# Kernel optimization log

Hardware: AMD Instinct MI355X
Metric: run time of the kernel (lower is better)

Reference implementation:

```python
import jax, jax.numpy as jnp
import numpy as np

DIM = 768
HEADS = 12
HIDDEN = int(DIM * 4.0)


def layernorm(x, w, b, eps=1e-5):
    mu = jnp.mean(x, axis=-1, keepdims=True)
    var = jnp.var(x, axis=-1, keepdims=True)
    return (x - mu) * jax.lax.rsqrt(var + eps) * w + b


def setup_inputs() -> dict:
    key = jax.random.key(0)
    ks = jax.random.split(key, 16)
    B, Nq, Nc, D = 4, 1024, 1024, DIM
    s = 0.02
    return {
        "query_tokens": jax.random.normal(ks[0], (B, Nq, D), jnp.float32),
        "context_tokens": jax.random.normal(ks[1], (B, Nc, D), jnp.float32),
        "wind_bias": jax.random.normal(ks[2], (B, 1, Nq, Nc), jnp.float32),
        "ln_q_w": jnp.ones((D,), jnp.float32), "ln_q_b": jnp.zeros((D,), jnp.float32),
        "ln_kv_w": jnp.ones((D,), jnp.float32), "ln_kv_b": jnp.zeros((D,), jnp.float32),
        "Wq": jax.random.normal(ks[3], (D, D), jnp.float32) * s, "bq": jnp.zeros((D,), jnp.float32),
        "Wk": jax.random.normal(ks[4], (D, D), jnp.float32) * s, "bk": jnp.zeros((D,), jnp.float32),
        "Wv": jax.random.normal(ks[5], (D, D), jnp.float32) * s, "bv": jnp.zeros((D,), jnp.float32),
        "Wo": jax.random.normal(ks[6], (D, D), jnp.float32) * s, "bo": jnp.zeros((D,), jnp.float32),
        "beta": jnp.ones((HEADS, 1, 1), jnp.float32),
        "ln_f_w": jnp.ones((D,), jnp.float32), "ln_f_b": jnp.zeros((D,), jnp.float32),
        "W1": jax.random.normal(ks[7], (D, HIDDEN), jnp.float32) * s, "b1": jnp.zeros((HIDDEN,), jnp.float32),
        "W2": jax.random.normal(ks[8], (HIDDEN, D), jnp.float32) * s, "b2": jnp.zeros((D,), jnp.float32),
    }


def reference(query_tokens, context_tokens, wind_bias,
              ln_q_w, ln_q_b, ln_kv_w, ln_kv_b,
              Wq, bq, Wk, bk, Wv, bv, Wo, bo, beta,
              ln_f_w, ln_f_b, W1, b1, W2, b2):
    B, Nq, D = query_tokens.shape
    H = HEADS
    hd = D // H
    scale = hd ** -0.5

    q = layernorm(query_tokens, ln_q_w, ln_q_b) @ Wq + bq
    kv = layernorm(context_tokens, ln_kv_w, ln_kv_b)
    k = kv @ Wk + bk
    v = kv @ Wv + bv

    # [B, H, N, hd]
    q = q.reshape(B, Nq, H, hd).transpose(0, 2, 1, 3)
    k = k.reshape(B, -1, H, hd).transpose(0, 2, 1, 3)
    v = v.reshape(B, -1, H, hd).transpose(0, 2, 1, 3)

    attn = jnp.einsum('bhqd,bhkd->bhqk', q * scale, k)
    attn = attn + beta * wind_bias  # beta: [H,1,1] broadcasts over [B,H,Nq,Nc]
    attn = jax.nn.softmax(attn.astype(jnp.float32), axis=-1).astype(q.dtype)

    out = jnp.einsum('bhqk,bhkd->bhqd', attn, v).transpose(0, 2, 1, 3).reshape(B, Nq, D)
    out = out @ Wo + bo

    x = query_tokens + out
    h = layernorm(x, ln_f_w, ln_f_b)
    h = jax.nn.gelu(h @ W1 + b1, approximate=False) @ W2 + b2
    return x + h
```

## Files before the change

kernel.cpp:

```cpp
#include <hip/hip_runtime.h>
#include <hip/hip_bf16.h>


#define DIM 768
#define HID 3072
#define NHEAD 12
#define BATCH 4
#define SEQ 1024
#define ROWS (BATCH * SEQ)
#define HD 64

typedef __attribute__((ext_vector_type(8))) __bf16 bf16x8;
typedef __attribute__((ext_vector_type(4))) float f32x4;
typedef __attribute__((ext_vector_type(4))) unsigned int u32x4;
typedef __attribute__((ext_vector_type(2))) unsigned int u32x2;

#define MFMA16(a, b, c) __builtin_amdgcn_mfma_f32_16x16x32_bf16((a), (b), (c), 0, 0, 0)

#define GLDS16(g, l)                                                         \
  __builtin_amdgcn_global_load_lds(                                          \
      (const __attribute__((address_space(1))) void*)(g),                    \
      (__attribute__((address_space(3))) void*)(l), 16, 0, 0)

__device__ __forceinline__ unsigned pk2(float lo, float hi) {
  unsigned a = __bfloat16_as_ushort(__float2bfloat16(lo));
  unsigned b = __bfloat16_as_ushort(__float2bfloat16(hi));
  return a | (b << 16);
}

__global__ __launch_bounds__(256) void wg_transpose4(const float* __restrict__ Wq,
                                                     const float* __restrict__ Wk,
                                                     const float* __restrict__ Wv,
                                                     const float* __restrict__ Wo,
                                                     __hip_bfloat16* __restrict__ WqT,
                                                     __hip_bfloat16* __restrict__ WkT,
                                                     __hip_bfloat16* __restrict__ WvT,
                                                     __hip_bfloat16* __restrict__ WoT) {
  __shared__ float tile[32][33];
  const int z = blockIdx.z;
  const float* W = (z == 0) ? Wq : (z == 1) ? Wk : (z == 2) ? Wv : Wo;
  __hip_bfloat16* WT = (z == 0) ? WqT : (z == 1) ? WkT : (z == 2) ? WvT : WoT;
  const int tx = threadIdx.x & 31, ty = threadIdx.x >> 5;
  const int n0 = blockIdx.x * 32, k0 = blockIdx.y * 32;
#pragma unroll
  for (int i = 0; i < 4; i++)
    tile[ty + i * 8][tx] = W[(size_t)(k0 + ty + i * 8) * DIM + n0 + tx];
  __syncthreads();
#pragma unroll
  for (int i = 0; i < 4; i++)
    WT[(size_t)(n0 + ty + i * 8) * DIM + k0 + tx] = __float2bfloat16(tile[tx][ty + i * 8]);
}

__global__ __launch_bounds__(256) void wg_transpose(const float* __restrict__ W,
                                                    __hip_bfloat16* __restrict__ WT,
                                                    int K, int N) {
  __shared__ float tile[32][33];
  const int tx = threadIdx.x & 31, ty = threadIdx.x >> 5;
  const int n0 = blockIdx.x * 32, k0 = blockIdx.y * 32;
#pragma unroll
  for (int i = 0; i < 4; i++)
    tile[ty + i * 8][tx] = W[(size_t)(k0 + ty + i * 8) * N + n0 + tx];
  __syncthreads();
#pragma unroll
  for (int i = 0; i < 4; i++)
    WT[(size_t)(n0 + ty + i * 8) * K + k0 + tx] = __float2bfloat16(tile[tx][ty + i * 8]);
}

__global__ void wg_bcat(const float* __restrict__ bq, const float* __restrict__ bk,
                        const float* __restrict__ bv, float* __restrict__ bc) {
  int i = blockIdx.x * 256 + threadIdx.x;
  if (i < 768) bc[i] = bq[i];
  else if (i < 1536) bc[i] = bk[i - 768];
  else if (i < 2304) bc[i] = bv[i - 1536];
}

template <int DUAL>
__global__ __launch_bounds__(256) void wg_ln(const float* __restrict__ inA,
                                             const float* __restrict__ wA,
                                             const float* __restrict__ bA,
                                             const float* __restrict__ inB,
                                             const float* __restrict__ wB,
                                             const float* __restrict__ bB,
                                             __hip_bfloat16* __restrict__ outbuf) {
  int row = blockIdx.x;
  int t = threadIdx.x;
  const float* in = inA;
  const float* w = wA;
  const float* b = bA;
  int lrow = row;
  if (DUAL && row >= ROWS) {
    in = inB; w = wB; b = bB; lrow = row - ROWS;
  }
  const float* p = in + (size_t)lrow * DIM;
  float v0 = p[t], v1 = p[t + 256], v2 = p[t + 512];
  float s = v0 + v1 + v2;
  float q = v0 * v0 + v1 * v1 + v2 * v2;
#pragma unroll
  for (int d = 1; d < 64; d <<= 1) {
    s += __shfl_xor(s, d);
    q += __shfl_xor(q, d);
  }
  __shared__ float ss[4], sq[4];
  if ((t & 63) == 0) {
    ss[t >> 6] = s;
    sq[t >> 6] = q;
  }
  __syncthreads();
  s = ss[0] + ss[1] + ss[2] + ss[3];
  q = sq[0] + sq[1] + sq[2] + sq[3];
  float mu = s * (1.0f / DIM);
  float var = q * (1.0f / DIM) - mu * mu;
  float rs = rsqrtf(var + 1e-5f);
  __hip_bfloat16* o = outbuf + (size_t)row * DIM;
  o[t] = __float2bfloat16((v0 - mu) * rs * w[t] + b[t]);
  o[t + 256] = __float2bfloat16((v1 - mu) * rs * w[t + 256] + b[t + 256]);
  o[t + 512] = __float2bfloat16((v2 - mu) * rs * w[t + 512] + b[t + 512]);
}

template <int MODE>
__global__ __launch_bounds__(512) void wg_gemm(const __hip_bfloat16* __restrict__ A,
                                               const __hip_bfloat16* __restrict__ BT,
                                               const float* __restrict__ bias,
                                               void* __restrict__ Cout,
                                               const float* __restrict__ resid,
                                               float* __restrict__ aux,
                                               int N, int Kloop, int Kstride, float p0) {
  __shared__ __hip_bfloat16 As[3][128 * 32];
  __shared__ __hip_bfloat16 Bs[3][128 * 32];
  const int t = threadIdx.x;
  const int lane = t & 63;
  const int wave = t >> 6;
  const int wr = wave >> 1, wc = wave & 1;
  const int lhi = lane >> 4, llo = lane & 15;
  const int nbn = N >> 7;
  const int bm = blockIdx.x / nbn, bn = blockIdx.x % nbn;
  const int koff = (MODE == 7) ? blockIdx.y * Kloop : 0;

  const __hip_bfloat16* Ause = A;
  if (MODE == 6 && bn >= 6) Ause = A + (size_t)ROWS * DIM;

  const int srow = t >> 2;
  const int sg = ((t & 3) ^ ((srow >> 1) & 3)) * 8;
  const __hip_bfloat16* Ag = Ause + (size_t)(bm * 128 + srow) * Kstride + koff + sg;
  const __hip_bfloat16* Bg = BT + (size_t)(bn * 128 + srow) * Kstride + koff + sg;

  f32x4 zero = {0.f, 0.f, 0.f, 0.f};
  f32x4 acc[2][4];
#pragma unroll
  for (int i = 0; i < 2; i++)
#pragma unroll
    for (int j = 0; j < 4; j++) acc[i][j] = zero;

  const int nk = Kloop >> 5;

  GLDS16(Ag, &As[0][t * 8]);
  GLDS16(Bg, &Bs[0][t * 8]);
  GLDS16(Ag + 32, &As[1][t * 8]);
  GLDS16(Bg + 32, &Bs[1][t * 8]);

  int buf = 0;
  for (int kt = 0; kt < nk; kt++) {
    if (kt < nk - 1) {
      asm volatile("s_waitcnt vmcnt(2)" ::: "memory");
    } else {
      asm volatile("s_waitcnt vmcnt(0)" ::: "memory");
    }
    __builtin_amdgcn_s_barrier();
    asm volatile("" ::: "memory");
    if (kt + 2 < nk) {
      int nbuf = buf + 2;
      if (nbuf >= 3) nbuf -= 3;
      GLDS16(Ag + (kt + 2) * 32, &As[nbuf][t * 8]);
      GLDS16(Bg + (kt + 2) * 32, &Bs[nbuf][t * 8]);
    }
    bf16x8 af[2], bfr[4];
#pragma unroll
    for (int i = 0; i < 2; i++) {
      const int row = wr * 32 + i * 16 + llo;
      af[i] = *reinterpret_cast<const bf16x8*>(
          &As[buf][row * 32 + ((lhi ^ ((row >> 1) & 3)) << 3)]);
    }
#pragma unroll
    for (int j = 0; j < 4; j++) {
      const int row = wc * 64 + j * 16 + llo;
      bfr[j] = *reinterpret_cast<const bf16x8*>(
          &Bs[buf][row * 32 + ((lhi ^ ((row >> 1) & 3)) << 3)]);
    }
    __builtin_amdgcn_s_setprio(1);
#pragma unroll
    for (int i = 0; i < 2; i++)
#pragma unroll
      for (int j = 0; j < 4; j++) acc[i][j] = MFMA16(af[i], bfr[j], acc[i][j]);
    __builtin_amdgcn_s_setprio(0);
    buf++;
    if (buf == 3) buf = 0;
  }

#pragma unroll
  for (int i = 0; i < 2; i++) {
    int gr = bm * 128 + wr * 32 + i * 16 + lhi * 4;
#pragma unroll
    for (int j = 0; j < 4; j++) {
      int gc = bn * 128 + wc * 64 + j * 16 + llo;
      float bv_ = (MODE == 7) ? 0.f : bias[gc];
#pragma unroll
      for (int r = 0; r < 4; r++) {
        float v = acc[i][j][r] + bv_;
        int row = gr + r;
        size_t idx = (size_t)row * N + gc;
        if (MODE == 3) {
          aux[idx] = resid[idx] + v;
        } else if (MODE == 4) {
          float x3 = v * v * v;
          float z = -2.302208f * v - 0.102943f * x3;
          float g = v / (1.0f + exp2f(z));
          ((__hip_bfloat16*)Cout)[idx] = __float2bfloat16(g);
        } else if (MODE == 7) {
          aux[(size_t)blockIdx.y * ROWS * N + idx] = v;
        } else if (MODE == 6) {
          int sec = gc / 768;
          int n2 = gc - sec * 768;
          __hip_bfloat16* base = (__hip_bfloat16*)Cout;
          if (sec == 0) {
            base[(size_t)row * DIM + n2] = __float2bfloat16(v * p0);
          } else if (sec == 1) {
            base[(size_t)ROWS * DIM + (size_t)row * DIM + n2] = __float2bfloat16(v);
          } else {
            int b_ = row >> 10, n_ = row & 1023;
            int h_ = n2 >> 6, d_ = n2 & 63;
            base[(size_t)2 * ROWS * DIM +
                 (((size_t)(b_ * NHEAD + h_) * HD + d_) << 10) + n_] = __float2bfloat16(v);
          }
        }
      }
    }
  }
}

template <int NP>
__global__ __launch_bounds__(256) void wg_red(const float* __restrict__ partial,
                                              const float* __restrict__ resid,
                                              const float* __restrict__ bias,
                                              float* __restrict__ out) {
  const int i = blockIdx.x * 256 + threadIdx.x;
  const int NF4 = ROWS * DIM / 4;
  if (i >= NF4) return;
  const f32x4* P = (const f32x4*)partial;
  f32x4 p = P[i];
#pragma unroll
  for (int c = 1; c < NP; c++) p += P[i + c * NF4];
  f32x4 r = ((const f32x4*)resid)[i];
  f32x4 bv = ((const f32x4*)bias)[i % (DIM / 4)];
  ((f32x4*)out)[i] = r + p + bv;
}

__global__ __launch_bounds__(256) void wg_attn4(const __hip_bfloat16* __restrict__ Q,
                                                const __hip_bfloat16* __restrict__ Kb,
                                                const __hip_bfloat16* __restrict__ Vt,
                                                const float* __restrict__ wb,
                                                const float* __restrict__ beta,
                                                __hip_bfloat16* __restrict__ O) {
  __shared__ __hip_bfloat16 Ks[2][4096];
  __shared__ __hip_bfloat16 Vs[2][4096];
  const int t = threadIdx.x;
  const int lane = t & 63;
  const int lhi = lane >> 4, llo = lane & 15;

  const int bid = blockIdx.x;
  const int wid = (bid & 7) * 96 + (bid >> 3);
  const int h = wid % NHEAD;
  const int g = wid / NHEAD;
  const int qt = g & 15;
  const int b = g >> 4;
  const float betah = beta[h] * 1.44269504089f;

  const int w = t >> 6;
  const size_t qrow0 = (size_t)b * SEQ + qt * 64 + w * 16;
  const __hip_bfloat16* Qp = Q + qrow0 * DIM + h * HD;
  bf16x8 a0 = *reinterpret_cast<const bf16x8*>(&Qp[(size_t)llo * DIM + lhi * 8]);
  bf16x8 a1 = *reinterpret_cast<const bf16x8*>(&Qp[(size_t)llo * DIM + 32 + lhi * 8]);

  const __hip_bfloat16* Kg = Kb + (size_t)b * SEQ * DIM + h * HD;
  const __hip_bfloat16* Vg = Vt + (size_t)(b * NHEAD + h) * HD * SEQ;
  const float* wrow = wb + (qrow0 + llo) * SEQ;

  const int slot0 = t, slot1 = t + 256;
  const int r0 = slot0 >> 3, c0 = (slot0 & 7) ^ (r0 & 7);
  const int r1 = slot1 >> 3, c1 = (slot1 & 7) ^ (r1 & 7);

  auto stage = [&](int buf, int kb) {
    GLDS16(Kg + (size_t)(kb + r0) * DIM + c0 * 8, &Ks[buf][slot0 * 8]);
    GLDS16(Kg + (size_t)(kb + r1) * DIM + c1 * 8, &Ks[buf][slot1 * 8]);
    GLDS16(Vg + (size_t)r0 * SEQ + kb + c0 * 8, &Vs[buf][slot0 * 8]);
    GLDS16(Vg + (size_t)r1 * SEQ + kb + c1 * 8, &Vs[buf][slot1 * 8]);
  };

  f32x4 zero = {0.f, 0.f, 0.f, 0.f};
  f32x4 oc[4];
#pragma unroll
  for (int c = 0; c < 4; c++) oc[c] = zero;
  float m_ = -1e30f, l_ = 0.f;

  f32x4 wv[4];
#pragma unroll
  for (int c2 = 0; c2 < 4; c2++)
    wv[c2] = *reinterpret_cast<const f32x4*>(&wrow[c2 * 16 + lhi * 4]);

  stage(0, 0);
  __syncthreads();
  int cur = 0;

  const int srcA = (lane & 15) | ((lane & 16) << 1);
  const bool chi = (lane & 32) != 0;

  for (int kt = 0; kt < SEQ / 64; kt++) {
    const int kb = kt * 64;
    f32x4 wvn[4];
    if (kt < SEQ / 64 - 1) {
      stage(cur ^ 1, kb + 64);
#pragma unroll
      for (int c2 = 0; c2 < 4; c2++)
        wvn[c2] = *reinterpret_cast<const f32x4*>(&wrow[kb + 64 + c2 * 16 + lhi * 4]);
    }

    f32x4 sv[4];
    __builtin_amdgcn_s_setprio(1);
#pragma unroll
    for (int c2 = 0; c2 < 4; c2++) {
      const int row = c2 * 16 + llo;
      bf16x8 k0 = *reinterpret_cast<const bf16x8*>(
          &Ks[cur][((row << 3) + (lhi ^ (row & 7))) << 3]);
      bf16x8 k1 = *reinterpret_cast<const bf16x8*>(
          &Ks[cur][((row << 3) + ((4 + lhi) ^ (row & 7))) << 3]);
      f32x4 s_ = zero;
      s_ = MFMA16(k0, a0, s_);
      s_ = MFMA16(k1, a1, s_);
      sv[c2] = s_;
    }
    __builtin_amdgcn_s_setprio(0);

#pragma unroll
    for (int c2 = 0; c2 < 4; c2++)
#pragma unroll
      for (int r = 0; r < 4; r++) sv[c2][r] += betah * wv[c2][r];

    float mx;
    {
      f32x4 m4;
#pragma unroll
      for (int r = 0; r < 4; r++)
        m4[r] = fmaxf(fmaxf(sv[0][r], sv[1][r]), fmaxf(sv[2][r], sv[3][r]));
      mx = fmaxf(fmaxf(m4[0], m4[1]), fmaxf(m4[2], m4[3]));
      mx = fmaxf(mx, __shfl_xor(mx, 16));
      mx = fmaxf(mx, __shfl_xor(mx, 32));
    }

    const bool grow = __any(mx > m_);
    float corr = 1.f;
    if (grow) {
      float mn = fmaxf(m_, mx);
      corr = exp2f(m_ - mn);
      m_ = mn;
    }

#pragma unroll
    for (int c2 = 0; c2 < 4; c2++)
#pragma unroll
      for (int r = 0; r < 4; r++) sv[c2][r] = exp2f(sv[c2][r] - m_);
    f32x4 s4;
#pragma unroll
    for (int r = 0; r < 4; r++) s4[r] = (sv[0][r] + sv[1][r]) + (sv[2][r] + sv[3][r]);
    float rs = (s4[0] + s4[1]) + (s4[2] + s4[3]);
    rs += __shfl_xor(rs, 16);
    rs += __shfl_xor(rs, 32);
    l_ = l_ * corr + rs;

    if (grow) {
      float cr[4];
#pragma unroll
      for (int r = 0; r < 4; r++) cr[r] = __shfl(corr, lhi * 4 + r);
#pragma unroll
      for (int c = 0; c < 4; c++)
#pragma unroll
        for (int r = 0; r < 4; r++) oc[c][r] *= cr[r];
    }

    unsigned p01[4], p23[4];
#pragma unroll
    for (int c2 = 0; c2 < 4; c2++) {
      p01[c2] = pk2(sv[c2][0], sv[c2][1]);
      p23[c2] = pk2(sv[c2][2], sv[c2][3]);
    }
    unsigned a01_0A = (unsigned)__shfl((int)p01[0], srcA);
    unsigned a01_1A = (unsigned)__shfl((int)p01[1], srcA);
    unsigned a23_0A = (unsigned)__shfl((int)p23[0], srcA);
    unsigned a23_1A = (unsigned)__shfl((int)p23[1], srcA);
    unsigned a01_0B = (unsigned)__shfl((int)p01[0], srcA + 16);
    unsigned a01_1B = (unsigned)__shfl((int)p01[1], srcA + 16);
    unsigned a23_0B = (unsigned)__shfl((int)p23[0], srcA + 16);
    unsigned a23_1B = (unsigned)__shfl((int)p23[1], srcA + 16);
    unsigned b01_2A = (unsigned)__shfl((int)p01[2], srcA);
    unsigned b01_3A = (unsigned)__shfl((int)p01[3], srcA);
    unsigned b23_2A = (unsigned)__shfl((int)p23[2], srcA);
    unsigned b23_3A = (unsigned)__shfl((int)p23[3], srcA);
    unsigned b01_2B = (unsigned)__shfl((int)p01[2], srcA + 16);
    unsigned b01_3B = (unsigned)__shfl((int)p01[3], srcA + 16);
    unsigned b23_2B = (unsigned)__shfl((int)p23[2], srcA + 16);
    unsigned b23_3B = (unsigned)__shfl((int)p23[3], srcA + 16);
    u32x4 t0, t1;
    t0[0] = chi ? a01_1A : a01_0A;
    t0[1] = chi ? a23_1A : a23_0A;
    t0[2] = chi ? a01_1B : a01_0B;
    t0[3] = chi ? a23_1B : a23_0B;
    t1[0] = chi ? b01_3A : b01_2A;
    t1[1] = chi ? b23_3A : b23_2A;
    t1[2] = chi ? b01_3B : b01_2B;
    t1[3] = chi ? b23_3B : b23_2B;
    bf16x8 pf0 = __builtin_bit_cast(bf16x8, t0);
    bf16x8 pf1 = __builtin_bit_cast(bf16x8, t1);

    __builtin_amdgcn_s_setprio(1);
#pragma unroll
    for (int c = 0; c < 4; c++) {
      const int row = c * 16 + llo;
      bf16x8 v0 = *reinterpret_cast<const bf16x8*>(
          &Vs[cur][((row << 3) + (lhi ^ (row & 7))) << 3]);
      bf16x8 v1 = *reinterpret_cast<const bf16x8*>(
          &Vs[cur][((row << 3) + ((4 + lhi) ^ (row & 7))) << 3]);
      oc[c] = MFMA16(pf0, v0, oc[c]);
      oc[c] = MFMA16(pf1, v1, oc[c]);
    }
    __builtin_amdgcn_s_setprio(0);

    if (kt < SEQ / 64 - 1) {
#pragma unroll
      for (int c2 = 0; c2 < 4; c2++) wv[c2] = wvn[c2];
    }
    __syncthreads();
    cur ^= 1;
  }

  float iv[4];
  float invl = 1.0f / l_;
#pragma unroll
  for (int r = 0; r < 4; r++) iv[r] = __shfl(invl, lhi * 4 + r);
  __hip_bfloat16* Op = O + qrow0 * DIM + h * HD;
#pragma unroll
  for (int c = 0; c < 4; c++)
#pragma unroll
    for (int r = 0; r < 4; r++)
      Op[(size_t)(lhi * 4 + r) * DIM + c * 16 + llo] = __float2bfloat16(oc[c][r] * iv[r]);
}

extern "C" void kernel_launch(void* const* d_in, const int* in_sizes, int n_in,
                              void* d_out, int out_size, void* d_ws, size_t ws_size,
                              hipStream_t stream) {
  const float* query = (const float*)d_in[0];
  const float* context = (const float*)d_in[1];
  const float* wind = (const float*)d_in[2];
  const float* ln_q_w = (const float*)d_in[3];
  const float* ln_q_b = (const float*)d_in[4];
  const float* ln_kv_w = (const float*)d_in[5];
  const float* ln_kv_b = (const float*)d_in[6];
  const float* Wq = (const float*)d_in[7];
  const float* bq = (const float*)d_in[8];
  const float* Wk = (const float*)d_in[9];
  const float* bk = (const float*)d_in[10];
  const float* Wv = (const float*)d_in[11];
  const float* bv = (const float*)d_in[12];
  const float* Wo = (const float*)d_in[13];
  const float* bo = (const float*)d_in[14];
  const float* beta = (const float*)d_in[15];
  const float* ln_f_w = (const float*)d_in[16];
  const float* ln_f_b = (const float*)d_in[17];
  const float* W1 = (const float*)d_in[18];
  const float* b1 = (const float*)d_in[19];
  const float* W2 = (const float*)d_in[20];
  const float* b2 = (const float*)d_in[21];
  float* out = (float*)d_out;

  char* ws = (char*)d_ws;
  size_t off = 0;
  auto take = [&](size_t bytes) -> char* {
    char* p = ws + off;
    off += (bytes + 255) & ~(size_t)255;
    return p;
  };
  const size_t actB = (size_t)ROWS * DIM * 2;
  __hip_bfloat16* qln = (__hip_bfloat16*)take(actB);
  __hip_bfloat16* kvln = (__hip_bfloat16*)take(actB);
  __hip_bfloat16* qb = (__hip_bfloat16*)take(actB);
  __hip_bfloat16* kbuf = (__hip_bfloat16*)take(actB);
  __hip_bfloat16* vt = (__hip_bfloat16*)take(actB);
  __hip_bfloat16* aout = (__hip_bfloat16*)take(actB);
  __hip_bfloat16* hbuf = (__hip_bfloat16*)take(actB);
  float* xbuf = (float*)take((size_t)ROWS * DIM * 4);
  __hip_bfloat16* hid = (__hip_bfloat16*)take((size_t)ROWS * HID * 2);
  __hip_bfloat16* WqT = (__hip_bfloat16*)take((size_t)DIM * DIM * 2);
  __hip_bfloat16* WkT = (__hip_bfloat16*)take((size_t)DIM * DIM * 2);
  __hip_bfloat16* WvT = (__hip_bfloat16*)take((size_t)DIM * DIM * 2);
  __hip_bfloat16* WoT = (__hip_bfloat16*)take((size_t)DIM * DIM * 2);
  __hip_bfloat16* W1T = (__hip_bfloat16*)take((size_t)DIM * HID * 2);
  __hip_bfloat16* W2T = (__hip_bfloat16*)take((size_t)HID * DIM * 2);
  float* bcat = (float*)take(2304 * 4);
  float* kpart = (float*)take((size_t)4 * ROWS * DIM * 4);

  wg_transpose4<<<dim3(24, 24, 4), 256, 0, stream>>>(Wq, Wk, Wv, Wo, WqT, WkT, WvT, WoT);
  wg_transpose<<<dim3(96, 24), 256, 0, stream>>>(W1, W1T, DIM, HID);
  wg_transpose<<<dim3(24, 96), 256, 0, stream>>>(W2, W2T, HID, DIM);
  wg_bcat<<<9, 256, 0, stream>>>(bq, bk, bv, bcat);

  wg_ln<1><<<2 * ROWS, 256, 0, stream>>>(query, ln_q_w, ln_q_b,
                                         context, ln_kv_w, ln_kv_b, qln);

  const float scale = 0.125f * 1.44269504089f;
  wg_gemm<6><<<32 * 18, 512, 0, stream>>>(qln, WqT, bcat, qb, nullptr, nullptr,
                                          2304, DIM, DIM, scale);

  wg_attn4<<<768, 256, 0, stream>>>(qb, kbuf, vt, wind, beta, aout);

  const int g768 = (ROWS / 128) * (DIM / 128);
  const int g3072 = (ROWS / 128) * (HID / 128);
  wg_gemm<3><<<g768, 512, 0, stream>>>(aout, WoT, bo, nullptr, query, xbuf, DIM, DIM, DIM, 0.f);
  wg_ln<0><<<ROWS, 256, 0, stream>>>(xbuf, ln_f_w, ln_f_b, nullptr, nullptr, nullptr, hbuf);
  wg_gemm<4><<<g3072, 512, 0, stream>>>(hbuf, W1T, b1, hid, nullptr, nullptr, HID, DIM, DIM, 0.f);
  wg_gemm<7><<<dim3(g768, 4), 512, 0, stream>>>(hid, W2T, nullptr, nullptr, nullptr, kpart,
                                                DIM, HID / 4, HID, 0.f);
  wg_red<4><<<(ROWS * DIM / 4 + 255) / 256, 256, 0, stream>>>(kpart, xbuf, b2, out);
}
```

Baseline: 215.4 us.

## Rewrite attention kernel with 32x32 MFMA tiles and two-wave blocks

Replaces the 16x16x32 MFMA attention with 32x32x16 MFMA tiles, so each wave handles 32 query rows and a block of 128 threads covers 64 queries. Softmax row reductions need one fewer cross-lane shuffle, and packing P into the B operand uses a single xor-32 shuffle instead of many indexed shuffles. The output is now staged through LDS for coalesced 16-byte global stores. In exchange each wave holds larger accumulator and score registers, and the block has half as many waves to hide latency.

```diff
diff --git a/kernel.cpp b/kernel.cpp
--- a/kernel.cpp
+++ b/kernel.cpp
@@ -12,10 +12,11 @@
 
 typedef __attribute__((ext_vector_type(8))) __bf16 bf16x8;
 typedef __attribute__((ext_vector_type(4))) float f32x4;
+typedef __attribute__((ext_vector_type(16))) float f32x16;
 typedef __attribute__((ext_vector_type(4))) unsigned int u32x4;
-typedef __attribute__((ext_vector_type(2))) unsigned int u32x2;
 
 #define MFMA16(a, b, c) __builtin_amdgcn_mfma_f32_16x16x32_bf16((a), (b), (c), 0, 0, 0)
+#define MFMA32(a, b, c) __builtin_amdgcn_mfma_f32_32x32x16_bf16((a), (b), (c), 0, 0, 0)
 
 #define GLDS16(g, l)                                                         \
   __builtin_amdgcn_global_load_lds(                                          \
@@ -254,17 +255,37 @@
   ((f32x4*)out)[i] = r + p + bv;
 }
 
-__global__ __launch_bounds__(256) void wg_attn4(const __hip_bfloat16* __restrict__ Q,
+#define PACKG(S, G2, OUT)                                                     \
+  {                                                                           \
+    unsigned pA0 = pk2((S)[8 * (G2) + 0], (S)[8 * (G2) + 1]);                 \
+    unsigned pA1 = pk2((S)[8 * (G2) + 2], (S)[8 * (G2) + 3]);                 \
+    unsigned pB0 = pk2((S)[8 * (G2) + 4], (S)[8 * (G2) + 5]);                 \
+    unsigned pB1 = pk2((S)[8 * (G2) + 6], (S)[8 * (G2) + 7]);                 \
+    unsigned u0 = l5 ? pB0 : pA0, v0 = l5 ? pA0 : pB0;                        \
+    unsigned u1 = l5 ? pB1 : pA1, v1 = l5 ? pA1 : pB1;                        \
+    unsigned w0 = (unsigned)__shfl_xor((int)v0, 32);                          \
+    unsigned w1 = (unsigned)__shfl_xor((int)v1, 32);                          \
+    u32x4 tb_;                                                                \
+    tb_[0] = l5 ? w0 : u0;                                                    \
+    tb_[1] = l5 ? w1 : u1;                                                    \
+    tb_[2] = l5 ? u0 : w0;                                                    \
+    tb_[3] = l5 ? u1 : w1;                                                    \
+    OUT = __builtin_bit_cast(bf16x8, tb_);                                    \
+  }
+
+__global__ __launch_bounds__(128) void wg_attn6(const __hip_bfloat16* __restrict__ Q,
                                                 const __hip_bfloat16* __restrict__ Kb,
                                                 const __hip_bfloat16* __restrict__ Vt,
                                                 const float* __restrict__ wb,
                                                 const float* __restrict__ beta,
                                                 __hip_bfloat16* __restrict__ O) {
-  __shared__ __hip_bfloat16 Ks[2][4096];
-  __shared__ __hip_bfloat16 Vs[2][4096];
+  __shared__ __align__(16) __hip_bfloat16 Ks[2][4096];
+  __shared__ __align__(16) __hip_bfloat16 Vs[2][4096];
   const int t = threadIdx.x;
   const int lane = t & 63;
-  const int lhi = lane >> 4, llo = lane & 15;
+  const int w = t >> 6;
+  const int l5 = lane >> 5;
+  const int l31 = lane & 31;
 
   const int bid = blockIdx.x;
   const int wid = (bid & 7) * 96 + (bid >> 3);
@@ -274,84 +295,98 @@
   const int b = g >> 4;
   const float betah = beta[h] * 1.44269504089f;
 
-  const int w = t >> 6;
-  const size_t qrow0 = (size_t)b * SEQ + qt * 64 + w * 16;
-  const __hip_bfloat16* Qp = Q + qrow0 * DIM + h * HD;
-  bf16x8 a0 = *reinterpret_cast<const bf16x8*>(&Qp[(size_t)llo * DIM + lhi * 8]);
-  bf16x8 a1 = *reinterpret_cast<const bf16x8*>(&Qp[(size_t)llo * DIM + 32 + lhi * 8]);
+  const int qrow0 = b * SEQ + qt * 64 + w * 32;
+  const __hip_bfloat16* Qp = Q + (size_t)(qrow0 + l31) * DIM + h * HD + l5 * 8;
+  bf16x8 qf[4];
+#pragma unroll
+  for (int hc = 0; hc < 4; hc++)
+    qf[hc] = *reinterpret_cast<const bf16x8*>(&Qp[hc * 16]);
 
   const __hip_bfloat16* Kg = Kb + (size_t)b * SEQ * DIM + h * HD;
   const __hip_bfloat16* Vg = Vt + (size_t)(b * NHEAD + h) * HD * SEQ;
-  const float* wrow = wb + (qrow0 + llo) * SEQ;
-
-  const int slot0 = t, slot1 = t + 256;
-  const int r0 = slot0 >> 3, c0 = (slot0 & 7) ^ (r0 & 7);
-  const int r1 = slot1 >> 3, c1 = (slot1 & 7) ^ (r1 & 7);
-
+  const float* wrow = wb + (size_t)(qrow0 + l31) * SEQ + l5 * 4;
+
+  int sr[4], sc[4];
+#pragma unroll
+  for (int i = 0; i < 4; i++) {
+    int s = t + 128 * i;
+    sr[i] = s >> 3;
+    sc[i] = ((s & 7) ^ (sr[i] & 7)) * 8;
+  }
   auto stage = [&](int buf, int kb) {
-    GLDS16(Kg + (size_t)(kb + r0) * DIM + c0 * 8, &Ks[buf][slot0 * 8]);
-    GLDS16(Kg + (size_t)(kb + r1) * DIM + c1 * 8, &Ks[buf][slot1 * 8]);
-    GLDS16(Vg + (size_t)r0 * SEQ + kb + c0 * 8, &Vs[buf][slot0 * 8]);
-    GLDS16(Vg + (size_t)r1 * SEQ + kb + c1 * 8, &Vs[buf][slot1 * 8]);
+#pragma unroll
+    for (int i = 0; i < 4; i++) {
+      GLDS16(Kg + (size_t)(kb + sr[i]) * DIM + sc[i], &Ks[buf][(t + 128 * i) * 8]);
+      GLDS16(Vg + (size_t)sr[i] * SEQ + kb + sc[i], &Vs[buf][(t + 128 * i) * 8]);
+    }
   };
 
-  f32x4 zero = {0.f, 0.f, 0.f, 0.f};
-  f32x4 oc[4];
-#pragma unroll
-  for (int c = 0; c < 4; c++) oc[c] = zero;
+  f32x16 oc0, oc1;
+#pragma unroll
+  for (int i = 0; i < 16; i++) {
+    oc0[i] = 0.f;
+    oc1[i] = 0.f;
+  }
   float m_ = -1e30f, l_ = 0.f;
 
-  f32x4 wv[4];
-#pragma unroll
-  for (int c2 = 0; c2 < 4; c2++)
-    wv[c2] = *reinterpret_cast<const f32x4*>(&wrow[c2 * 16 + lhi * 4]);
+  f32x4 wv[8];
+#pragma unroll
+  for (int i = 0; i < 8; i++) wv[i] = *reinterpret_cast<const f32x4*>(&wrow[i * 8]);
 
   stage(0, 0);
   __syncthreads();
   int cur = 0;
 
-  const int srcA = (lane & 15) | ((lane & 16) << 1);
-  const bool chi = (lane & 32) != 0;
-
-  for (int kt = 0; kt < SEQ / 64; kt++) {
+  for (int kt = 0; kt < 16; kt++) {
     const int kb = kt * 64;
-    f32x4 wvn[4];
-    if (kt < SEQ / 64 - 1) {
-      stage(cur ^ 1, kb + 64);
-#pragma unroll
-      for (int c2 = 0; c2 < 4; c2++)
-        wvn[c2] = *reinterpret_cast<const f32x4*>(&wrow[kb + 64 + c2 * 16 + lhi * 4]);
-    }
-
-    f32x4 sv[4];
+    if (kt < 15) stage(cur ^ 1, kb + 64);
+
+    f32x16 s0, s1;
+#pragma unroll
+    for (int i = 0; i < 16; i++) {
+      s0[i] = 0.f;
+      s1[i] = 0.f;
+    }
     __builtin_amdgcn_s_setprio(1);
 #pragma unroll
-    for (int c2 = 0; c2 < 4; c2++) {
-      const int row = c2 * 16 + llo;
-      bf16x8 k0 = *reinterpret_cast<const bf16x8*>(
-          &Ks[cur][((row << 3) + (lhi ^ (row & 7))) << 3]);
-      bf16x8 k1 = *reinterpret_cast<const bf16x8*>(
-          &Ks[cur][((row << 3) + ((4 + lhi) ^ (row & 7))) << 3]);
-      f32x4 s_ = zero;
-      s_ = MFMA16(k0, a0, s_);
-      s_ = MFMA16(k1, a1, s_);
-      sv[c2] = s_;
+    for (int hc = 0; hc < 4; hc++) {
+      const int row = l31;
+      bf16x8 kf = *reinterpret_cast<const bf16x8*>(
+          &Ks[cur][row * 64 + (((hc * 2 + l5) ^ (row & 7)) << 3)]);
+      s0 = MFMA32(kf, qf[hc], s0);
+    }
+#pragma unroll
+    for (int hc = 0; hc < 4; hc++) {
+      const int row = 32 + l31;
+      bf16x8 kf = *reinterpret_cast<const bf16x8*>(
+          &Ks[cur][row * 64 + (((hc * 2 + l5) ^ (row & 7)) << 3)]);
+      s1 = MFMA32(kf, qf[hc], s1);
     }
     __builtin_amdgcn_s_setprio(0);
 
 #pragma unroll
-    for (int c2 = 0; c2 < 4; c2++)
-#pragma unroll
-      for (int r = 0; r < 4; r++) sv[c2][r] += betah * wv[c2][r];
+    for (int rq = 0; rq < 4; rq++)
+#pragma unroll
+      for (int rb = 0; rb < 4; rb++) {
+        s0[4 * rq + rb] += betah * wv[rq][rb];
+        s1[4 * rq + rb] += betah * wv[rq + 4][rb];
+      }
+    if (kt < 15) {
+#pragma unroll
+      for (int i = 0; i < 8; i++)
+        wv[i] = *reinterpret_cast<const f32x4*>(&wrow[kb + 64 + i * 8]);
+    }
 
     float mx;
     {
       f32x4 m4;
 #pragma unroll
-      for (int r = 0; r < 4; r++)
-        m4[r] = fmaxf(fmaxf(sv[0][r], sv[1][r]), fmaxf(sv[2][r], sv[3][r]));
+      for (int r = 0; r < 4; r++) {
+        float a_ = fmaxf(fmaxf(s0[r], s0[4 + r]), fmaxf(s0[8 + r], s0[12 + r]));
+        float b_ = fmaxf(fmaxf(s1[r], s1[4 + r]), fmaxf(s1[8 + r], s1[12 + r]));
+        m4[r] = fmaxf(a_, b_);
+      }
       mx = fmaxf(fmaxf(m4[0], m4[1]), fmaxf(m4[2], m4[3]));
-      mx = fmaxf(mx, __shfl_xor(mx, 16));
       mx = fmaxf(mx, __shfl_xor(mx, 32));
     }
 
@@ -363,93 +398,75 @@
       m_ = mn;
     }
 
-#pragma unroll
-    for (int c2 = 0; c2 < 4; c2++)
-#pragma unroll
-      for (int r = 0; r < 4; r++) sv[c2][r] = exp2f(sv[c2][r] - m_);
-    f32x4 s4;
-#pragma unroll
-    for (int r = 0; r < 4; r++) s4[r] = (sv[0][r] + sv[1][r]) + (sv[2][r] + sv[3][r]);
-    float rs = (s4[0] + s4[1]) + (s4[2] + s4[3]);
-    rs += __shfl_xor(rs, 16);
+    float rs = 0.f;
+#pragma unroll
+    for (int i = 0; i < 16; i++) {
+      s0[i] = exp2f(s0[i] - m_);
+      s1[i] = exp2f(s1[i] - m_);
+      rs += s0[i] + s1[i];
+    }
     rs += __shfl_xor(rs, 32);
     l_ = l_ * corr + rs;
 
     if (grow) {
-      float cr[4];
-#pragma unroll
-      for (int r = 0; r < 4; r++) cr[r] = __shfl(corr, lhi * 4 + r);
-#pragma unroll
-      for (int c = 0; c < 4; c++)
-#pragma unroll
-        for (int r = 0; r < 4; r++) oc[c][r] *= cr[r];
-    }
-
-    unsigned p01[4], p23[4];
-#pragma unroll
-    for (int c2 = 0; c2 < 4; c2++) {
-      p01[c2] = pk2(sv[c2][0], sv[c2][1]);
-      p23[c2] = pk2(sv[c2][2], sv[c2][3]);
-    }
-    unsigned a01_0A = (unsigned)__shfl((int)p01[0], srcA);
-    unsigned a01_1A = (unsigned)__shfl((int)p01[1], srcA);
-    unsigned a23_0A = (unsigned)__shfl((int)p23[0], srcA);
-    unsigned a23_1A = (unsigned)__shfl((int)p23[1], srcA);
-    unsigned a01_0B = (unsigned)__shfl((int)p01[0], srcA + 16);
-    unsigned a01_1B = (unsigned)__shfl((int)p01[1], srcA + 16);
-    unsigned a23_0B = (unsigned)__shfl((int)p23[0], srcA + 16);
-    unsigned a23_1B = (unsigned)__shfl((int)p23[1], srcA + 16);
-    unsigned b01_2A = (unsigned)__shfl((int)p01[2], srcA);
-    unsigned b01_3A = (unsigned)__shfl((int)p01[3], srcA);
-    unsigned b23_2A = (unsigned)__shfl((int)p23[2], srcA);
-    unsigned b23_3A = (unsigned)__shfl((int)p23[3], srcA);
-    unsigned b01_2B = (unsigned)__shfl((int)p01[2], srcA + 16);
-    unsigned b01_3B = (unsigned)__shfl((int)p01[3], srcA + 16);
-    unsigned b23_2B = (unsigned)__shfl((int)p23[2], srcA + 16);
-    unsigned b23_3B = (unsigned)__shfl((int)p23[3], srcA + 16);
-    u32x4 t0, t1;
-    t0[0] = chi ? a01_1A : a01_0A;
-    t0[1] = chi ? a23_1A : a23_0A;
-    t0[2] = chi ? a01_1B : a01_0B;
-    t0[3] = chi ? a23_1B : a23_0B;
-    t1[0] = chi ? b01_3A : b01_2A;
-    t1[1] = chi ? b23_3A : b23_2A;
-    t1[2] = chi ? b01_3B : b01_2B;
-    t1[3] = chi ? b23_3B : b23_2B;
-    bf16x8 pf0 = __builtin_bit_cast(bf16x8, t0);
-    bf16x8 pf1 = __builtin_bit_cast(bf16x8, t1);
+#pragma unroll
+      for (int i = 0; i < 16; i++) {
+        oc0[i] *= corr;
+        oc1[i] *= corr;
+      }
+    }
+
+    bf16x8 pb0, pb1, pb2, pb3;
+    PACKG(s0, 0, pb0);
+    PACKG(s0, 1, pb1);
+    PACKG(s1, 0, pb2);
+    PACKG(s1, 1, pb3);
 
     __builtin_amdgcn_s_setprio(1);
 #pragma unroll
-    for (int c = 0; c < 4; c++) {
-      const int row = c * 16 + llo;
-      bf16x8 v0 = *reinterpret_cast<const bf16x8*>(
-          &Vs[cur][((row << 3) + (lhi ^ (row & 7))) << 3]);
-      bf16x8 v1 = *reinterpret_cast<const bf16x8*>(
-          &Vs[cur][((row << 3) + ((4 + lhi) ^ (row & 7))) << 3]);
-      oc[c] = MFMA16(pf0, v0, oc[c]);
-      oc[c] = MFMA16(pf1, v1, oc[c]);
+    for (int gi = 0; gi < 4; gi++) {
+      const bf16x8 pb = (gi == 0) ? pb0 : (gi == 1) ? pb1 : (gi == 2) ? pb2 : pb3;
+      {
+        const int row = l31;
+        bf16x8 vf = *reinterpret_cast<const bf16x8*>(
+            &Vs[cur][row * 64 + (((gi * 2 + l5) ^ (row & 7)) << 3)]);
+        oc0 = MFMA32(vf, pb, oc0);
+      }
+      {
+        const int row = 32 + l31;
+        bf16x8 vf = *reinterpret_cast<const bf16x8*>(
+            &Vs[cur][row * 64 + (((gi * 2 + l5) ^ (row & 7)) << 3)]);
+        oc1 = MFMA32(vf, pb, oc1);
+      }
     }
     __builtin_amdgcn_s_setprio(0);
 
-    if (kt < SEQ / 64 - 1) {
-#pragma unroll
-      for (int c2 = 0; c2 < 4; c2++) wv[c2] = wvn[c2];
-    }
     __syncthreads();
     cur ^= 1;
   }
 
-  float iv[4];
-  float invl = 1.0f / l_;
-#pragma unroll
-  for (int r = 0; r < 4; r++) iv[r] = __shfl(invl, lhi * 4 + r);
-  __hip_bfloat16* Op = O + qrow0 * DIM + h * HD;
-#pragma unroll
-  for (int c = 0; c < 4; c++)
-#pragma unroll
-    for (int r = 0; r < 4; r++)
-      Op[(size_t)(lhi * 4 + r) * DIM + c * 16 + llo] = __float2bfloat16(oc[c][r] * iv[r]);
+  const float inv = 1.0f / l_;
+  unsigned* tbuf = (unsigned*)((w == 0) ? (void*)&Ks[0][0] : (void*)&Vs[0][0]);
+#pragma unroll
+  for (int rq = 0; rq < 4; rq++) {
+    unsigned a0 = pk2(oc0[4 * rq + 0] * inv, oc0[4 * rq + 1] * inv);
+    unsigned a1 = pk2(oc0[4 * rq + 2] * inv, oc0[4 * rq + 3] * inv);
+    unsigned b0 = pk2(oc1[4 * rq + 0] * inv, oc1[4 * rq + 1] * inv);
+    unsigned b1 = pk2(oc1[4 * rq + 2] * inv, oc1[4 * rq + 3] * inv);
+    tbuf[l31 * 36 + 4 * rq + 2 * l5 + 0] = a0;
+    tbuf[l31 * 36 + 4 * rq + 2 * l5 + 1] = a1;
+    tbuf[l31 * 36 + 4 * rq + 2 * l5 + 16] = b0;
+    tbuf[l31 * 36 + 4 * rq + 2 * l5 + 17] = b1;
+  }
+  asm volatile("s_waitcnt lgkmcnt(0)" ::: "memory");
+  unsigned* outp = (unsigned*)O;
+  const int q_ = lane >> 1, hf = lane & 1;
+#pragma unroll
+  for (int i = 0; i < 4; i++) {
+    u32x4 vv = *reinterpret_cast<const u32x4*>(&tbuf[q_ * 36 + hf * 16 + i * 4]);
+    *reinterpret_cast<u32x4*>(
+        &outp[(size_t)(qrow0 + q_) * 384 + h * 32 + hf * 16 + i * 4]) = vv;
+  }
 }
 
 extern "C" void kernel_launch(void* const* d_in, const int* in_sizes, int n_in,
@@ -517,7 +534,7 @@
   wg_gemm<6><<<32 * 18, 512, 0, stream>>>(qln, WqT, bcat, qb, nullptr, nullptr,
                                           2304, DIM, DIM, scale);
 
-  wg_attn4<<<768, 256, 0, stream>>>(qb, kbuf, vt, wind, beta, aout);
+  wg_attn6<<<768, 128, 0, stream>>>(qb, kbuf, vt, wind, beta, aout);
 
   const int g768 = (ROWS / 128) * (DIM / 128);
   const int g3072 = (ROWS / 128) * (HID / 128);
```

Result: slower. 221.2 us (+2.7%).

## Split attention over two KV halves and merge partials in a combine kernel

Applied to the files above, without the earlier changes.

The attention kernel now splits the key/value sequence in two along a second grid dimension, doubling the block count from 768 to 1536. Each block writes unnormalized fp32 partial outputs plus running max and sum to a workspace. A new combine kernel rescales and merges the two halves into the bf16 attention output. This targets under-occupancy of the GPU's compute units with only 768 blocks, at the cost of extra fp32 partial traffic and an additional kernel launch.

```diff
diff --git a/kernel.cpp b/kernel.cpp
--- a/kernel.cpp
+++ b/kernel.cpp
@@ -9,11 +9,11 @@
 #define SEQ 1024
 #define ROWS (BATCH * SEQ)
 #define HD 64
+#define NBH (BATCH * NHEAD)
 
 typedef __attribute__((ext_vector_type(8))) __bf16 bf16x8;
 typedef __attribute__((ext_vector_type(4))) float f32x4;
 typedef __attribute__((ext_vector_type(4))) unsigned int u32x4;
-typedef __attribute__((ext_vector_type(2))) unsigned int u32x2;
 
 #define MFMA16(a, b, c) __builtin_amdgcn_mfma_f32_16x16x32_bf16((a), (b), (c), 0, 0, 0)
 
@@ -254,17 +254,20 @@
   ((f32x4*)out)[i] = r + p + bv;
 }
 
-__global__ __launch_bounds__(256) void wg_attn4(const __hip_bfloat16* __restrict__ Q,
+__global__ __launch_bounds__(256) void wg_attn7(const __hip_bfloat16* __restrict__ Q,
                                                 const __hip_bfloat16* __restrict__ Kb,
                                                 const __hip_bfloat16* __restrict__ Vt,
                                                 const float* __restrict__ wb,
                                                 const float* __restrict__ beta,
-                                                __hip_bfloat16* __restrict__ O) {
+                                                float* __restrict__ apart,
+                                                float* __restrict__ astat) {
   __shared__ __hip_bfloat16 Ks[2][4096];
   __shared__ __hip_bfloat16 Vs[2][4096];
   const int t = threadIdx.x;
   const int lane = t & 63;
   const int lhi = lane >> 4, llo = lane & 15;
+  const int kz = blockIdx.y;
+  const int kv0 = kz * (SEQ / 2);
 
   const int bid = blockIdx.x;
   const int wid = (bid & 7) * 96 + (bid >> 3);
@@ -304,19 +307,20 @@
   f32x4 wv[4];
 #pragma unroll
   for (int c2 = 0; c2 < 4; c2++)
-    wv[c2] = *reinterpret_cast<const f32x4*>(&wrow[c2 * 16 + lhi * 4]);
-
-  stage(0, 0);
+    wv[c2] = *reinterpret_cast<const f32x4*>(&wrow[kv0 + c2 * 16 + lhi * 4]);
+
+  stage(0, kv0);
   __syncthreads();
   int cur = 0;
 
   const int srcA = (lane & 15) | ((lane & 16) << 1);
   const bool chi = (lane & 32) != 0;
 
-  for (int kt = 0; kt < SEQ / 64; kt++) {
-    const int kb = kt * 64;
+  const int NT = SEQ / 2 / 64;
+  for (int kt = 0; kt < NT; kt++) {
+    const int kb = kv0 + kt * 64;
     f32x4 wvn[4];
-    if (kt < SEQ / 64 - 1) {
+    if (kt < NT - 1) {
       stage(cur ^ 1, kb + 64);
 #pragma unroll
       for (int c2 = 0; c2 < 4; c2++)
@@ -432,7 +436,7 @@
     }
     __builtin_amdgcn_s_setprio(0);
 
-    if (kt < SEQ / 64 - 1) {
+    if (kt < NT - 1) {
 #pragma unroll
       for (int c2 = 0; c2 < 4; c2++) wv[c2] = wvn[c2];
     }
@@ -440,16 +444,42 @@
     cur ^= 1;
   }
 
-  float iv[4];
-  float invl = 1.0f / l_;
-#pragma unroll
-  for (int r = 0; r < 4; r++) iv[r] = __shfl(invl, lhi * 4 + r);
-  __hip_bfloat16* Op = O + qrow0 * DIM + h * HD;
+  float* po = apart + (size_t)kz * ROWS * DIM + qrow0 * DIM + h * HD;
 #pragma unroll
   for (int c = 0; c < 4; c++)
 #pragma unroll
     for (int r = 0; r < 4; r++)
-      Op[(size_t)(lhi * 4 + r) * DIM + c * 16 + llo] = __float2bfloat16(oc[c][r] * iv[r]);
+      po[(size_t)(lhi * 4 + r) * DIM + c * 16 + llo] = oc[c][r];
+  if (lhi == 0) {
+    const int idx = (b * NHEAD + h) * SEQ + qt * 64 + w * 16 + llo;
+    astat[(kz * 2 + 0) * (NBH * SEQ) + idx] = m_;
+    astat[(kz * 2 + 1) * (NBH * SEQ) + idx] = l_;
+  }
+}
+
+__global__ __launch_bounds__(256) void wg_acomb(const float* __restrict__ apart,
+                                                const float* __restrict__ astat,
+                                                __hip_bfloat16* __restrict__ aout) {
+  const int row = blockIdx.x;
+  const int t = threadIdx.x;
+  const int b = row >> 10, n = row & 1023;
+  const float* p0 = apart + (size_t)row * DIM;
+  const float* p1 = apart + (size_t)ROWS * DIM + (size_t)row * DIM;
+  __hip_bfloat16* o = aout + (size_t)row * DIM;
+#pragma unroll
+  for (int i = 0; i < 3; i++) {
+    const int col = t + i * 256;
+    const int h = col >> 6;
+    const int si = (b * NHEAD + h) * SEQ + n;
+    float m0 = astat[si];
+    float l0 = astat[NBH * SEQ + si];
+    float m1 = astat[2 * NBH * SEQ + si];
+    float l1 = astat[3 * NBH * SEQ + si];
+    float mf = fmaxf(m0, m1);
+    float w0 = exp2f(m0 - mf), w1 = exp2f(m1 - mf);
+    float inv = 1.0f / (l0 * w0 + l1 * w1);
+    o[col] = __float2bfloat16((p0[col] * w0 + p1[col] * w1) * inv);
+  }
 }
 
 extern "C" void kernel_launch(void* const* d_in, const int* in_sizes, int n_in,
@@ -504,6 +534,8 @@
   __hip_bfloat16* W2T = (__hip_bfloat16*)take((size_t)HID * DIM * 2);
   float* bcat = (float*)take(2304 * 4);
   float* kpart = (float*)take((size_t)4 * ROWS * DIM * 4);
+  float* apart = kpart;
+  float* astat = kpart + (size_t)2 * ROWS * DIM;
 
   wg_transpose4<<<dim3(24, 24, 4), 256, 0, stream>>>(Wq, Wk, Wv, Wo, WqT, WkT, WvT, WoT);
   wg_transpose<<<dim3(96, 24), 256, 0, stream>>>(W1, W1T, DIM, HID);
@@ -517,7 +549,8 @@
   wg_gemm<6><<<32 * 18, 512, 0, stream>>>(qln, WqT, bcat, qb, nullptr, nullptr,
                                           2304, DIM, DIM, scale);
 
-  wg_attn4<<<768, 256, 0, stream>>>(qb, kbuf, vt, wind, beta, aout);
+  wg_attn7<<<dim3(768, 2), 256, 0, stream>>>(qb, kbuf, vt, wind, beta, apart, astat);
+  wg_acomb<<<ROWS, 256, 0, stream>>>(apart, astat, aout);
 
   const int g768 = (ROWS / 128) * (DIM / 128);
   const int g3072 = (ROWS / 128) * (HID / 128);
```

After: 227.9 us. +5.8%, slower.

## Triple-buffer attention K/V/bias loads and split-K the output projection

Applied to the files above, without the earlier changes.

The attention kernel moves from double to triple buffering of K, V and the wind-bias registers. Loads are issued two tiles ahead, and the per-tile __syncthreads is replaced by a vmcnt wait plus a barrier, with occupancy hinted at 3 blocks. The Wo projection GEMM now runs as a 2-way split-K into partial buffers, followed by a reduction kernel that adds the residual and bias. This targets load latency in attention and the low block count of the 768-wide GEMM, at the cost of more LDS and registers per block and an extra kernel launch with partial-sum traffic.

```diff
diff --git a/kernel.cpp b/kernel.cpp
--- a/kernel.cpp
+++ b/kernel.cpp
@@ -13,7 +13,6 @@
 typedef __attribute__((ext_vector_type(8))) __bf16 bf16x8;
 typedef __attribute__((ext_vector_type(4))) float f32x4;
 typedef __attribute__((ext_vector_type(4))) unsigned int u32x4;
-typedef __attribute__((ext_vector_type(2))) unsigned int u32x2;
 
 #define MFMA16(a, b, c) __builtin_amdgcn_mfma_f32_16x16x32_bf16((a), (b), (c), 0, 0, 0)
 
@@ -208,9 +207,7 @@
         float v = acc[i][j][r] + bv_;
         int row = gr + r;
         size_t idx = (size_t)row * N + gc;
-        if (MODE == 3) {
-          aux[idx] = resid[idx] + v;
-        } else if (MODE == 4) {
+        if (MODE == 4) {
           float x3 = v * v * v;
           float z = -2.302208f * v - 0.102943f * x3;
           float g = v / (1.0f + exp2f(z));
@@ -254,14 +251,14 @@
   ((f32x4*)out)[i] = r + p + bv;
 }
 
-__global__ __launch_bounds__(256) void wg_attn4(const __hip_bfloat16* __restrict__ Q,
-                                                const __hip_bfloat16* __restrict__ Kb,
-                                                const __hip_bfloat16* __restrict__ Vt,
-                                                const float* __restrict__ wb,
-                                                const float* __restrict__ beta,
-                                                __hip_bfloat16* __restrict__ O) {
-  __shared__ __hip_bfloat16 Ks[2][4096];
-  __shared__ __hip_bfloat16 Vs[2][4096];
+__global__ __launch_bounds__(256, 3) void wg_attn8(const __hip_bfloat16* __restrict__ Q,
+                                                   const __hip_bfloat16* __restrict__ Kb,
+                                                   const __hip_bfloat16* __restrict__ Vt,
+                                                   const float* __restrict__ wb,
+                                                   const float* __restrict__ beta,
+                                                   __hip_bfloat16* __restrict__ O) {
+  __shared__ __hip_bfloat16 Ks[3][4096];
+  __shared__ __hip_bfloat16 Vs[3][4096];
   const int t = threadIdx.x;
   const int lane = t & 63;
   const int lhi = lane >> 4, llo = lane & 15;
@@ -288,12 +285,7 @@
   const int r0 = slot0 >> 3, c0 = (slot0 & 7) ^ (r0 & 7);
   const int r1 = slot1 >> 3, c1 = (slot1 & 7) ^ (r1 & 7);
 
-  auto stage = [&](int buf, int kb) {
-    GLDS16(Kg + (size_t)(kb + r0) * DIM + c0 * 8, &Ks[buf][slot0 * 8]);
-    GLDS16(Kg + (size_t)(kb + r1) * DIM + c1 * 8, &Ks[buf][slot1 * 8]);
-    GLDS16(Vg + (size_t)r0 * SEQ + kb + c0 * 8, &Vs[buf][slot0 * 8]);
-    GLDS16(Vg + (size_t)r1 * SEQ + kb + c1 * 8, &Vs[buf][slot1 * 8]);
-  };
+  f32x4 wvb[3][4];
 
   f32x4 zero = {0.f, 0.f, 0.f, 0.f};
   f32x4 oc[4];
@@ -301,27 +293,35 @@
   for (int c = 0; c < 4; c++) oc[c] = zero;
   float m_ = -1e30f, l_ = 0.f;
 
-  f32x4 wv[4];
-#pragma unroll
-  for (int c2 = 0; c2 < 4; c2++)
-    wv[c2] = *reinterpret_cast<const f32x4*>(&wrow[c2 * 16 + lhi * 4]);
-
-  stage(0, 0);
-  __syncthreads();
-  int cur = 0;
-
   const int srcA = (lane & 15) | ((lane & 16) << 1);
   const bool chi = (lane & 32) != 0;
 
-  for (int kt = 0; kt < SEQ / 64; kt++) {
-    const int kb = kt * 64;
-    f32x4 wvn[4];
-    if (kt < SEQ / 64 - 1) {
-      stage(cur ^ 1, kb + 64);
-#pragma unroll
-      for (int c2 = 0; c2 < 4; c2++)
-        wvn[c2] = *reinterpret_cast<const f32x4*>(&wrow[kb + 64 + c2 * 16 + lhi * 4]);
-    }
+#define STAGEW(BUF, KB)                                                       \
+  {                                                                           \
+    GLDS16(Kg + (size_t)((KB) + r0) * DIM + c0 * 8, &Ks[BUF][slot0 * 8]);     \
+    GLDS16(Kg + (size_t)((KB) + r1) * DIM + c1 * 8, &Ks[BUF][slot1 * 8]);     \
+    GLDS16(Vg + (size_t)r0 * SEQ + (KB) + c0 * 8, &Vs[BUF][slot0 * 8]);       \
+    GLDS16(Vg + (size_t)r1 * SEQ + (KB) + c1 * 8, &Vs[BUF][slot1 * 8]);       \
+    _Pragma("unroll") for (int c2 = 0; c2 < 4; c2++) wvb[BUF][c2] =           \
+        *reinterpret_cast<const f32x4*>(&wrow[(KB) + c2 * 16 + lhi * 4]);     \
+  }
+
+  STAGEW(0, 0);
+  STAGEW(1, 64);
+
+#pragma unroll
+  for (int kt = 0; kt < 16; kt++) {
+    if (kt < 15) {
+      asm volatile("s_waitcnt vmcnt(8)" ::: "memory");
+    } else {
+      asm volatile("s_waitcnt vmcnt(0)" ::: "memory");
+    }
+    __builtin_amdgcn_s_barrier();
+    asm volatile("" ::: "memory");
+    if (kt + 2 < 16) {
+      STAGEW((kt + 2) % 3, (kt + 2) * 64);
+    }
+    const int cur = kt % 3;
 
     f32x4 sv[4];
     __builtin_amdgcn_s_setprio(1);
@@ -342,7 +342,7 @@
 #pragma unroll
     for (int c2 = 0; c2 < 4; c2++)
 #pragma unroll
-      for (int r = 0; r < 4; r++) sv[c2][r] += betah * wv[c2][r];
+      for (int r = 0; r < 4; r++) sv[c2][r] += betah * wvb[kt % 3][c2][r];
 
     float mx;
     {
@@ -431,14 +431,8 @@
       oc[c] = MFMA16(pf1, v1, oc[c]);
     }
     __builtin_amdgcn_s_setprio(0);
-
-    if (kt < SEQ / 64 - 1) {
-#pragma unroll
-      for (int c2 = 0; c2 < 4; c2++) wv[c2] = wvn[c2];
-    }
-    __syncthreads();
-    cur ^= 1;
-  }
+  }
+#undef STAGEW
 
   float iv[4];
   float invl = 1.0f / l_;
@@ -517,11 +511,14 @@
   wg_gemm<6><<<32 * 18, 512, 0, stream>>>(qln, WqT, bcat, qb, nullptr, nullptr,
                                           2304, DIM, DIM, scale);
 
-  wg_attn4<<<768, 256, 0, stream>>>(qb, kbuf, vt, wind, beta, aout);
+  wg_attn8<<<768, 256, 0, stream>>>(qb, kbuf, vt, wind, beta, aout);
 
   const int g768 = (ROWS / 128) * (DIM / 128);
   const int g3072 = (ROWS / 128) * (HID / 128);
-  wg_gemm<3><<<g768, 512, 0, stream>>>(aout, WoT, bo, nullptr, query, xbuf, DIM, DIM, DIM, 0.f);
+  wg_gemm<7><<<dim3(g768, 2), 512, 0, stream>>>(aout, WoT, nullptr, nullptr, nullptr,
+                                                kpart, DIM, DIM / 2, DIM, 0.f);
+  wg_red<2><<<(ROWS * DIM / 4 + 255) / 256, 256, 0, stream>>>(kpart, query, bo, xbuf);
+
   wg_ln<0><<<ROWS, 256, 0, stream>>>(xbuf, ln_f_w, ln_f_b, nullptr, nullptr, nullptr, hbuf);
   wg_gemm<4><<<g3072, 512, 0, stream>>>(hbuf, W1T, b1, hid, nullptr, nullptr, HID, DIM, DIM, 0.f);
   wg_gemm<7><<<dim3(g768, 4), 512, 0, stream>>>(hid, W2T, nullptr, nullptr, nullptr, kpart,
```

Result: no change. 218.0 us (+1.2%).
